# Kernel optimization log

Hardware: AMD Instinct MI355X
Metric: run time of the kernel (lower is better)

## Reference

```python
import jax, jax.numpy as jnp
import numpy as np

STD_MIN = 1e-05
MAX_VAL = 100.0

B, T, C = 16, 8192, 128


def setup_inputs() -> dict:
    key = jax.random.key(0)
    k1, k2 = jax.random.split(key)
    x = jax.random.normal(k1, (B, T, C), dtype=jnp.float32)
    # binary missing-value mask (1 = missing), stored as float per mask.float() in torch
    mask = jax.random.randint(k2, (B, T, C), 0, 2).astype(jnp.float32)
    return {"x": x, "mask": mask}


def reference(x, mask):
    # valid-count running along time: n_t = cumsum(1 - mask)
    nm = 1.0 - mask                      # [B,T,C], 1 where observed
    n = jnp.cumsum(nm, axis=1)
    n = jnp.where(n == 0, 1.0, n)        # avoid div-by-zero before first valid point
    # causal running mean (note: cumsum of x includes masked entries, as in original)
    mean = jax.lax.stop_gradient(jnp.cumsum(x, axis=1) / n)
    # causal running std over masked squared deviations
    std = jnp.sqrt(jnp.cumsum(((x - mean) * nm) ** 2, axis=1) / n)
    std = jnp.where(std > STD_MIN, std, 1.0)
    std = jax.lax.stop_gradient(std)
    return jnp.clip((x - mean) / std, -MAX_VAL, MAX_VAL)
```

## Files before the change

### kernel.cpp

```cpp
#include <hip/hip_runtime.h>
#include <math.h>

constexpr int B = 16;
constexpr int T = 8192;
constexpr int C = 128;
constexpr int CG = C / 4;
constexpr int LSUB = 32;
constexpr int NC = T / LSUB;
constexpr float STD_MIN = 1e-5f;
constexpr float MAX_VAL = 100.0f;

using f32x4 = __attribute__((ext_vector_type(4))) float;

__device__ inline f32x4 sel_neff(f32x4 n) {
    f32x4 r;
    #pragma unroll
    for (int j = 0; j < 4; ++j) r[j] = (n[j] == 0.0f) ? 1.0f : n[j];
    return r;
}
__device__ inline f32x4 rcp4(f32x4 a) {
    f32x4 r;
    #pragma unroll
    for (int j = 0; j < 4; ++j) r[j] = __builtin_amdgcn_rcpf(a[j]);
    return r;
}
__device__ inline f32x4 sqrt4(f32x4 a) {
    f32x4 r;
    #pragma unroll
    for (int j = 0; j < 4; ++j) r[j] = __builtin_amdgcn_sqrtf(a[j]);
    return r;
}
__device__ inline f32x4 decode_nm(unsigned w) {
    f32x4 r;
    #pragma unroll
    for (int j = 0; j < 4; ++j) r[j] = (float)((w >> (8 * j)) & 0xffu);
    return r;
}

__device__ inline void decomp(int gtid, int& b, int& k, int& cg) {
    cg = gtid & (CG - 1);
    k  = (gtid / CG) & (NC - 1);
    b  = gtid / (CG * NC);
}

template <bool BYTES>
__global__ __launch_bounds__(256) void k_pass1(
    const f32x4* __restrict__ x, const f32x4* __restrict__ mask,
    f32x4* __restrict__ sumx, f32x4* __restrict__ sumnm,
    unsigned* __restrict__ nmb)
{
    int gtid = blockIdx.x * 256 + threadIdx.x;
    int b, k, cg; decomp(gtid, b, k, cg);
    size_t base = ((size_t)b * T + (size_t)k * LSUB) * CG + cg;
    f32x4 sx = {0,0,0,0}, sn = {0,0,0,0};
    #pragma unroll 8
    for (int t = 0; t < LSUB; ++t) {
        f32x4 xv = x[base + (size_t)t * CG];
        f32x4 mv = mask[base + (size_t)t * CG];
        f32x4 nm = 1.0f - mv;
        if (BYTES) {
            unsigned w = (unsigned)nm[0] | ((unsigned)nm[1] << 8)
                       | ((unsigned)nm[2] << 16) | ((unsigned)nm[3] << 24);
            nmb[base + (size_t)t * CG] = w;
        }
        sx += xv;
        sn += nm;
    }
    size_t o = ((size_t)b * NC + k) * CG + cg;
    sumx[o]  = sx;
    sumnm[o] = sn;
}

template <int NCOMP>
__device__ inline void block_exscan(float* vals, int lane, int wave)
{
    float inc[NCOMP];
    #pragma unroll
    for (int j = 0; j < NCOMP; ++j) inc[j] = vals[j];
    #pragma unroll
    for (int d = 1; d < 64; d <<= 1) {
        #pragma unroll
        for (int j = 0; j < NCOMP; ++j) {
            float u = __shfl_up(inc[j], d, 64);
            if (lane >= d) inc[j] += u;
        }
    }
    __shared__ float wsum[4][NCOMP];
    if (lane == 63) {
        #pragma unroll
        for (int j = 0; j < NCOMP; ++j) wsum[wave][j] = inc[j];
    }
    __syncthreads();
    float off[NCOMP];
    #pragma unroll
    for (int j = 0; j < NCOMP; ++j) off[j] = 0.0f;
    for (int w = 0; w < wave; ++w) {
        #pragma unroll
        for (int j = 0; j < NCOMP; ++j) off[j] += wsum[w][j];
    }
    #pragma unroll
    for (int j = 0; j < NCOMP; ++j) {
        float e = __shfl_up(inc[j], 1, 64);
        vals[j] = off[j] + ((lane == 0) ? 0.0f : e);
    }
}

__global__ __launch_bounds__(256) void k_scan2(f32x4* __restrict__ a0,
                                               f32x4* __restrict__ a1)
{
    int blk = blockIdx.x, cg = blk & 31, b = blk >> 5;
    int k = threadIdx.x, lane = k & 63, wave = k >> 6;
    size_t o = ((size_t)b * NC + k) * CG + cg;
    f32x4 v0 = a0[o], v1 = a1[o];
    float vals[8] = {v0[0],v0[1],v0[2],v0[3],v1[0],v1[1],v1[2],v1[3]};
    block_exscan<8>(vals, lane, wave);
    a0[o] = (f32x4){vals[0],vals[1],vals[2],vals[3]};
    a1[o] = (f32x4){vals[4],vals[5],vals[6],vals[7]};
}

__global__ __launch_bounds__(256) void k_scan1(f32x4* __restrict__ a0)
{
    int blk = blockIdx.x, cg = blk & 31, b = blk >> 5;
    int k = threadIdx.x, lane = k & 63, wave = k >> 6;
    size_t o = ((size_t)b * NC + k) * CG + cg;
    f32x4 v0 = a0[o];
    float vals[4] = {v0[0],v0[1],v0[2],v0[3]};
    block_exscan<4>(vals, lane, wave);
    a0[o] = (f32x4){vals[0],vals[1],vals[2],vals[3]};
}

template <bool BYTES>
__global__ __launch_bounds__(256) void k_pass3(
    const f32x4* __restrict__ x, const f32x4* __restrict__ mask,
    const unsigned* __restrict__ nmb,
    const f32x4* __restrict__ psumx, const f32x4* __restrict__ psumnm,
    f32x4* __restrict__ sumd2)
{
    int gtid = blockIdx.x * 256 + threadIdx.x;
    int b, k, cg; decomp(gtid, b, k, cg);
    size_t base = ((size_t)b * T + (size_t)k * LSUB) * CG + cg;
    size_t o = ((size_t)b * NC + k) * CG + cg;
    f32x4 rx = psumx[o], rn = psumnm[o];
    f32x4 sd = {0,0,0,0};
    #pragma unroll 8
    for (int t = 0; t < LSUB; ++t) {
        f32x4 xv = x[base + (size_t)t * CG];
        f32x4 nm = BYTES ? decode_nm(nmb[base + (size_t)t * CG])
                         : (1.0f - mask[base + (size_t)t * CG]);
        rx += xv; rn += nm;
        f32x4 mean = rx * rcp4(sel_neff(rn));
        f32x4 d = (xv - mean) * nm;
        sd += d * d;
    }
    sumd2[o] = sd;
}

template <bool BYTES>
__global__ __launch_bounds__(256) void k_pass5(
    const f32x4* __restrict__ x, const f32x4* __restrict__ mask,
    const unsigned* __restrict__ nmb,
    const f32x4* __restrict__ psumx, const f32x4* __restrict__ psumnm,
    const f32x4* __restrict__ psumd2, f32x4* __restrict__ out)
{
    int gtid = blockIdx.x * 256 + threadIdx.x;
    int b, k, cg; decomp(gtid, b, k, cg);
    size_t base = ((size_t)b * T + (size_t)k * LSUB) * CG + cg;
    size_t o = ((size_t)b * NC + k) * CG + cg;
    f32x4 rx = psumx[o], rn = psumnm[o], rd = psumd2[o];
    #pragma unroll 8
    for (int t = 0; t < LSUB; ++t) {
        f32x4 xv = x[base + (size_t)t * CG];
        f32x4 nm = BYTES ? decode_nm(nmb[base + (size_t)t * CG])
                         : (1.0f - mask[base + (size_t)t * CG]);
        rx += xv; rn += nm;
        f32x4 inv = rcp4(sel_neff(rn));
        f32x4 mean = rx * inv;
        f32x4 d = (xv - mean) * nm;
        rd += d * d;
        f32x4 s = sqrt4(rd * inv);
        f32x4 ov;
        #pragma unroll
        for (int j = 0; j < 4; ++j) {
            float invs = (s[j] > STD_MIN) ? __builtin_amdgcn_rcpf(s[j]) : 1.0f;
            float v = (xv[j] - mean[j]) * invs;
            ov[j] = fminf(fmaxf(v, -MAX_VAL), MAX_VAL);
        }
        __builtin_nontemporal_store(ov, &out[base + (size_t)t * CG]);
    }
}

template <bool BYTES>
static void run_all(const f32x4* x, const f32x4* mask, f32x4* out,
                    void* d_ws, hipStream_t stream)
{
    size_t arr_elems = (size_t)B * NC * C;
    f32x4* sumx  = (f32x4*)d_ws;
    f32x4* sumnm = (f32x4*)((float*)d_ws + arr_elems);
    f32x4* sumd2 = (f32x4*)((float*)d_ws + 2 * arr_elems);
    unsigned* nmb = (unsigned*)((float*)d_ws + 3 * arr_elems);

    int main_blocks = B * NC * CG / 256;
    int scan_blocks = B * CG;

    k_pass1<BYTES><<<main_blocks, 256, 0, stream>>>(x, mask, sumx, sumnm, nmb);
    k_scan2<<<scan_blocks, 256, 0, stream>>>(sumx, sumnm);
    k_pass3<BYTES><<<main_blocks, 256, 0, stream>>>(x, mask, nmb, sumx, sumnm, sumd2);
    k_scan1<<<scan_blocks, 256, 0, stream>>>(sumd2);
    k_pass5<BYTES><<<main_blocks, 256, 0, stream>>>(x, mask, nmb, sumx, sumnm, sumd2, out);
}

extern "C" void kernel_launch(void* const* d_in, const int* in_sizes, int n_in,
                              void* d_out, int out_size, void* d_ws, size_t ws_size,
                              hipStream_t stream) {
    const f32x4* x    = (const f32x4*)d_in[0];
    const f32x4* mask = (const f32x4*)d_in[1];
    f32x4* out = (f32x4*)d_out;

    size_t need = 3ull * B * NC * C * sizeof(float)
                + (size_t)B * T * CG * sizeof(unsigned);

    if (ws_size >= need) run_all<true >(x, mask, out, d_ws, stream);
    else                 run_all<false>(x, mask, out, d_ws, stream);
}
```

Before: 87.26 us.

## Split pass1 into tile-cooperative x-sum and mask-sum kernels

Replaces the per-thread strided pass1 with two kernels in which each block covers one 32-step time tile. Threads read contiguous rows and reduce through shared memory, which should make the loads coalesced and better distributed. The mask kernel uses nontemporal loads so the mask stream avoids polluting cache, hoping x stays cached for the next pass. The cost is an extra kernel launch plus a shared-memory reduction and barrier per block.

```diff
diff --git a/kernel.cpp b/kernel.cpp
--- a/kernel.cpp
+++ b/kernel.cpp
@@ -5,8 +5,9 @@
 constexpr int T = 8192;
 constexpr int C = 128;
 constexpr int CG = C / 4;
-constexpr int LSUB = 32;
-constexpr int NC = T / LSUB;
+constexpr int TB = 32;
+constexpr int NC = T / TB;
+constexpr int LSUB = TB;
 constexpr float STD_MIN = 1e-5f;
 constexpr float MAX_VAL = 100.0f;
 
@@ -44,31 +45,56 @@
 }
 
 template <bool BYTES>
-__global__ __launch_bounds__(256) void k_pass1(
-    const f32x4* __restrict__ x, const f32x4* __restrict__ mask,
-    f32x4* __restrict__ sumx, f32x4* __restrict__ sumnm,
+__global__ __launch_bounds__(256) void k_p1a(
+    const f32x4* __restrict__ mask, f32x4* __restrict__ sumnm,
     unsigned* __restrict__ nmb)
 {
-    int gtid = blockIdx.x * 256 + threadIdx.x;
-    int b, k, cg; decomp(gtid, b, k, cg);
-    size_t base = ((size_t)b * T + (size_t)k * LSUB) * CG + cg;
-    f32x4 sx = {0,0,0,0}, sn = {0,0,0,0};
-    #pragma unroll 8
-    for (int t = 0; t < LSUB; ++t) {
-        f32x4 xv = x[base + (size_t)t * CG];
-        f32x4 mv = mask[base + (size_t)t * CG];
+    __shared__ f32x4 p[8][CG];
+    int tid = threadIdx.x, cg = tid & 31, sub = tid >> 5;
+    int blk = blockIdx.x, b = blk >> 8, kb = blk & 255;
+    size_t gbase = (size_t)(b * T + kb * TB) * CG;
+    f32x4 sn = {0,0,0,0};
+    #pragma unroll
+    for (int i = 0; i < 4; ++i) {
+        f32x4 mv;
+        if (BYTES) mv = __builtin_nontemporal_load(&mask[gbase + i * 256 + tid]);
+        else       mv = mask[gbase + i * 256 + tid];
         f32x4 nm = 1.0f - mv;
         if (BYTES) {
             unsigned w = (unsigned)nm[0] | ((unsigned)nm[1] << 8)
                        | ((unsigned)nm[2] << 16) | ((unsigned)nm[3] << 24);
-            nmb[base + (size_t)t * CG] = w;
+            nmb[gbase + i * 256 + tid] = w;
         }
-        sx += xv;
         sn += nm;
     }
-    size_t o = ((size_t)b * NC + k) * CG + cg;
-    sumx[o]  = sx;
-    sumnm[o] = sn;
+    p[sub][cg] = sn;
+    __syncthreads();
+    if (sub == 0) {
+        f32x4 t = p[0][cg];
+        #pragma unroll
+        for (int s = 1; s < 8; ++s) t += p[s][cg];
+        sumnm[((size_t)b * NC + kb) * CG + cg] = t;
+    }
+}
+
+__global__ __launch_bounds__(256) void k_p1b(
+    const f32x4* __restrict__ x, f32x4* __restrict__ sumx)
+{
+    __shared__ f32x4 p[8][CG];
+    int tid = threadIdx.x, cg = tid & 31, sub = tid >> 5;
+    int blk = blockIdx.x, b = blk >> 8, kb = blk & 255;
+    size_t gbase = (size_t)(b * T + kb * TB) * CG;
+    f32x4 sx = {0,0,0,0};
+    #pragma unroll
+    for (int i = 0; i < 4; ++i) sx += x[gbase + i * 256 + tid];
+    p[sub][cg] = sx;
+    __syncthreads();
+    if (sub == 0) {
+        f32x4 t = p[0][cg];
+        #pragma unroll
+        for (int s = 1; s < 8; ++s) t += p[s][cg];
+        sumx[((size_t)b * NC + kb) * CG + cg] = t;
+    }
 }
 
 template <int NCOMP>
@@ -199,10 +225,12 @@
     f32x4* sumd2 = (f32x4*)((float*)d_ws + 2 * arr_elems);
     unsigned* nmb = (unsigned*)((float*)d_ws + 3 * arr_elems);
 
+    int tile_blocks = B * NC;
     int main_blocks = B * NC * CG / 256;
     int scan_blocks = B * CG;
 
-    k_pass1<BYTES><<<main_blocks, 256, 0, stream>>>(x, mask, sumx, sumnm, nmb);
+    k_p1b<<<tile_blocks, 256, 0, stream>>>(x, sumx);
+    k_p1a<BYTES><<<tile_blocks, 256, 0, stream>>>(mask, sumnm, nmb);
     k_scan2<<<scan_blocks, 256, 0, stream>>>(sumx, sumnm);
     k_pass3<BYTES><<<main_blocks, 256, 0, stream>>>(x, mask, nmb, sumx, sumnm, sumd2);
     k_scan1<<<scan_blocks, 256, 0, stream>>>(sumd2);
```

Result: slower. 89.81 us (+2.9%).

## Fuse scans into passes, bit-pack mask, use 128-row chunks per block

Applied to the files above, without the earlier changes.

Replaces the five-kernel pipeline (two passes, two scan kernels, final pass) with three kernels. Each block covers a 128-row time chunk and computes its cross-chunk prefix by summing earlier chunk aggregates directly, so the separate scan kernels go away. The mask is packed to one bit per element in a 64-bit word instead of one byte, cutting mask traffic in the later passes. The cost is redundant prefix reads that grow with the chunk index, extra shared-memory syncs, and holding all 16 rows of x per thread in registers. The workspace-size fallback is removed.

```diff
diff --git a/kernel.cpp b/kernel.cpp
--- a/kernel.cpp
+++ b/kernel.cpp
@@ -1,12 +1,15 @@
 #include <hip/hip_runtime.h>
 #include <math.h>
+#include <stdint.h>
 
 constexpr int B = 16;
 constexpr int T = 8192;
 constexpr int C = 128;
 constexpr int CG = C / 4;
-constexpr int LSUB = 32;
-constexpr int NC = T / LSUB;
+constexpr int TBK = 128;
+constexpr int NCH = T / TBK;
+constexpr int SUBS = 8;
+constexpr int RPT = TBK / SUBS;
 constexpr float STD_MIN = 1e-5f;
 constexpr float MAX_VAL = 100.0f;
 
@@ -30,183 +33,184 @@
     for (int j = 0; j < 4; ++j) r[j] = __builtin_amdgcn_sqrtf(a[j]);
     return r;
 }
-__device__ inline f32x4 decode_nm(unsigned w) {
-    f32x4 r;
-    #pragma unroll
-    for (int j = 0; j < 4; ++j) r[j] = (float)((w >> (8 * j)) & 0xffu);
-    return r;
-}
-
-__device__ inline void decomp(int gtid, int& b, int& k, int& cg) {
-    cg = gtid & (CG - 1);
-    k  = (gtid / CG) & (NC - 1);
-    b  = gtid / (CG * NC);
-}
-
-template <bool BYTES>
-__global__ __launch_bounds__(256) void k_pass1(
+__device__ inline f32x4 decode_nib(unsigned nib) {
+    f32x4 r;
+    r[0] = (float)(nib & 1u);
+    r[1] = (float)((nib >> 1) & 1u);
+    r[2] = (float)((nib >> 2) & 1u);
+    r[3] = (float)((nib >> 3) & 1u);
+    return r;
+}
+
+__global__ __launch_bounds__(256) void k1_sums(
     const f32x4* __restrict__ x, const f32x4* __restrict__ mask,
-    f32x4* __restrict__ sumx, f32x4* __restrict__ sumnm,
-    unsigned* __restrict__ nmb)
+    f32x4* __restrict__ aggx, f32x4* __restrict__ aggn,
+    uint64_t* __restrict__ nmw)
 {
-    int gtid = blockIdx.x * 256 + threadIdx.x;
-    int b, k, cg; decomp(gtid, b, k, cg);
-    size_t base = ((size_t)b * T + (size_t)k * LSUB) * CG + cg;
+    __shared__ f32x4 p0[SUBS][CG], p1[SUBS][CG];
+    int tid = threadIdx.x, cg = tid & 31, sub = tid >> 5;
+    int blk = blockIdx.x, b = blk >> 6, k = blk & (NCH - 1);
+    size_t base = ((size_t)b * T + (size_t)k * TBK + (size_t)sub * RPT) * CG + cg;
+
     f32x4 sx = {0,0,0,0}, sn = {0,0,0,0};
-    #pragma unroll 8
-    for (int t = 0; t < LSUB; ++t) {
-        f32x4 xv = x[base + (size_t)t * CG];
-        f32x4 mv = mask[base + (size_t)t * CG];
+    uint64_t w = 0;
+    #pragma unroll
+    for (int r = 0; r < RPT; ++r) {
+        f32x4 xv = x[base + (size_t)r * CG];
+        f32x4 mv = mask[base + (size_t)r * CG];
         f32x4 nm = 1.0f - mv;
-        if (BYTES) {
-            unsigned w = (unsigned)nm[0] | ((unsigned)nm[1] << 8)
-                       | ((unsigned)nm[2] << 16) | ((unsigned)nm[3] << 24);
-            nmb[base + (size_t)t * CG] = w;
-        }
-        sx += xv;
-        sn += nm;
-    }
-    size_t o = ((size_t)b * NC + k) * CG + cg;
-    sumx[o]  = sx;
-    sumnm[o] = sn;
-}
-
-template <int NCOMP>
-__device__ inline void block_exscan(float* vals, int lane, int wave)
+        sx += xv; sn += nm;
+        unsigned nib = (unsigned)nm[0] | ((unsigned)nm[1] << 1)
+                     | ((unsigned)nm[2] << 2) | ((unsigned)nm[3] << 3);
+        w |= (uint64_t)nib << (4 * r);
+    }
+    nmw[(size_t)blk * 256 + tid] = w;
+    p0[sub][cg] = sx; p1[sub][cg] = sn;
+    __syncthreads();
+    if (sub == 0) {
+        f32x4 tx = p0[0][cg], tn = p1[0][cg];
+        #pragma unroll
+        for (int s = 1; s < SUBS; ++s) { tx += p0[s][cg]; tn += p1[s][cg]; }
+        aggx[(size_t)blk * CG + cg] = tx;
+        aggn[(size_t)blk * CG + cg] = tn;
+    }
+}
+
+__global__ __launch_bounds__(256) void k2_dev2(
+    const f32x4* __restrict__ x,
+    const f32x4* __restrict__ aggx, const f32x4* __restrict__ aggn,
+    const uint64_t* __restrict__ nmw, f32x4* __restrict__ aggd)
 {
-    float inc[NCOMP];
-    #pragma unroll
-    for (int j = 0; j < NCOMP; ++j) inc[j] = vals[j];
-    #pragma unroll
-    for (int d = 1; d < 64; d <<= 1) {
+    __shared__ f32x4 p0[SUBS][CG], p1[SUBS][CG];
+    int tid = threadIdx.x, cg = tid & 31, sub = tid >> 5;
+    int blk = blockIdx.x, b = blk >> 6, k = blk & (NCH - 1);
+    size_t base = ((size_t)b * T + (size_t)k * TBK + (size_t)sub * RPT) * CG + cg;
+
+    f32x4 pxp = {0,0,0,0}, pnp = {0,0,0,0};
+    for (int j = sub; j < k; j += SUBS) {
+        size_t o = ((size_t)(b * NCH + j)) * CG + cg;
+        pxp += aggx[o]; pnp += aggn[o];
+    }
+    p0[sub][cg] = pxp; p1[sub][cg] = pnp;
+    __syncthreads();
+    f32x4 px = p0[0][cg], pn = p1[0][cg];
+    #pragma unroll
+    for (int s = 1; s < SUBS; ++s) { px += p0[s][cg]; pn += p1[s][cg]; }
+
+    f32x4 xr[RPT];
+    #pragma unroll
+    for (int r = 0; r < RPT; ++r) xr[r] = x[base + (size_t)r * CG];
+    uint64_t w = nmw[(size_t)blk * 256 + tid];
+
+    f32x4 sx = {0,0,0,0}, sn = {0,0,0,0};
+    #pragma unroll
+    for (int r = 0; r < RPT; ++r) {
+        sx += xr[r];
+        sn += decode_nib((unsigned)(w >> (4 * r)) & 0xFu);
+    }
+    __syncthreads();
+    p0[sub][cg] = sx; p1[sub][cg] = sn;
+    __syncthreads();
+    f32x4 offx = {0,0,0,0}, offn = {0,0,0,0};
+    for (int s = 0; s < sub; ++s) { offx += p0[s][cg]; offn += p1[s][cg]; }
+
+    f32x4 rx = px + offx, rn = pn + offn, sd = {0,0,0,0};
+    #pragma unroll
+    for (int r = 0; r < RPT; ++r) {
+        f32x4 nm = decode_nib((unsigned)(w >> (4 * r)) & 0xFu);
+        rx += xr[r]; rn += nm;
+        f32x4 mean = rx * rcp4(sel_neff(rn));
+        f32x4 d = (xr[r] - mean) * nm;
+        sd += d * d;
+    }
+    __syncthreads();
+    p0[sub][cg] = sd;
+    __syncthreads();
+    if (sub == 0) {
+        f32x4 td = p0[0][cg];
         #pragma unroll
-        for (int j = 0; j < NCOMP; ++j) {
-            float u = __shfl_up(inc[j], d, 64);
-            if (lane >= d) inc[j] += u;
-        }
-    }
-    __shared__ float wsum[4][NCOMP];
-    if (lane == 63) {
-        #pragma unroll
-        for (int j = 0; j < NCOMP; ++j) wsum[wave][j] = inc[j];
-    }
-    __syncthreads();
-    float off[NCOMP];
-    #pragma unroll
-    for (int j = 0; j < NCOMP; ++j) off[j] = 0.0f;
-    for (int w = 0; w < wave; ++w) {
-        #pragma unroll
-        for (int j = 0; j < NCOMP; ++j) off[j] += wsum[w][j];
-    }
-    #pragma unroll
-    for (int j = 0; j < NCOMP; ++j) {
-        float e = __shfl_up(inc[j], 1, 64);
-        vals[j] = off[j] + ((lane == 0) ? 0.0f : e);
-    }
-}
-
-__global__ __launch_bounds__(256) void k_scan2(f32x4* __restrict__ a0,
-                                               f32x4* __restrict__ a1)
+        for (int s = 1; s < SUBS; ++s) td += p0[s][cg];
+        aggd[(size_t)blk * CG + cg] = td;
+    }
+}
+
+__global__ __launch_bounds__(256) void k3_final(
+    const f32x4* __restrict__ x,
+    const f32x4* __restrict__ aggx, const f32x4* __restrict__ aggn,
+    const f32x4* __restrict__ aggd, const uint64_t* __restrict__ nmw,
+    f32x4* __restrict__ out)
 {
-    int blk = blockIdx.x, cg = blk & 31, b = blk >> 5;
-    int k = threadIdx.x, lane = k & 63, wave = k >> 6;
-    size_t o = ((size_t)b * NC + k) * CG + cg;
-    f32x4 v0 = a0[o], v1 = a1[o];
-    float vals[8] = {v0[0],v0[1],v0[2],v0[3],v1[0],v1[1],v1[2],v1[3]};
-    block_exscan<8>(vals, lane, wave);
-    a0[o] = (f32x4){vals[0],vals[1],vals[2],vals[3]};
-    a1[o] = (f32x4){vals[4],vals[5],vals[6],vals[7]};
-}
-
-__global__ __launch_bounds__(256) void k_scan1(f32x4* __restrict__ a0)
-{
-    int blk = blockIdx.x, cg = blk & 31, b = blk >> 5;
-    int k = threadIdx.x, lane = k & 63, wave = k >> 6;
-    size_t o = ((size_t)b * NC + k) * CG + cg;
-    f32x4 v0 = a0[o];
-    float vals[4] = {v0[0],v0[1],v0[2],v0[3]};
-    block_exscan<4>(vals, lane, wave);
-    a0[o] = (f32x4){vals[0],vals[1],vals[2],vals[3]};
-}
-
-template <bool BYTES>
-__global__ __launch_bounds__(256) void k_pass3(
-    const f32x4* __restrict__ x, const f32x4* __restrict__ mask,
-    const unsigned* __restrict__ nmb,
-    const f32x4* __restrict__ psumx, const f32x4* __restrict__ psumnm,
-    f32x4* __restrict__ sumd2)
-{
-    int gtid = blockIdx.x * 256 + threadIdx.x;
-    int b, k, cg; decomp(gtid, b, k, cg);
-    size_t base = ((size_t)b * T + (size_t)k * LSUB) * CG + cg;
-    size_t o = ((size_t)b * NC + k) * CG + cg;
-    f32x4 rx = psumx[o], rn = psumnm[o];
-    f32x4 sd = {0,0,0,0};
-    #pragma unroll 8
-    for (int t = 0; t < LSUB; ++t) {
-        f32x4 xv = x[base + (size_t)t * CG];
-        f32x4 nm = BYTES ? decode_nm(nmb[base + (size_t)t * CG])
-                         : (1.0f - mask[base + (size_t)t * CG]);
-        rx += xv; rn += nm;
+    __shared__ f32x4 p0[SUBS][CG], p1[SUBS][CG], p2[SUBS][CG];
+    int tid = threadIdx.x, cg = tid & 31, sub = tid >> 5;
+    int blk = blockIdx.x, b = blk >> 6, k = blk & (NCH - 1);
+    size_t base = ((size_t)b * T + (size_t)k * TBK + (size_t)sub * RPT) * CG + cg;
+
+    f32x4 pxp = {0,0,0,0}, pnp = {0,0,0,0}, pdp = {0,0,0,0};
+    for (int j = sub; j < k; j += SUBS) {
+        size_t o = ((size_t)(b * NCH + j)) * CG + cg;
+        pxp += aggx[o]; pnp += aggn[o]; pdp += aggd[o];
+    }
+    p0[sub][cg] = pxp; p1[sub][cg] = pnp; p2[sub][cg] = pdp;
+    __syncthreads();
+    f32x4 px = p0[0][cg], pn = p1[0][cg], pd = p2[0][cg];
+    #pragma unroll
+    for (int s = 1; s < SUBS; ++s) {
+        px += p0[s][cg]; pn += p1[s][cg]; pd += p2[s][cg];
+    }
+
+    f32x4 xr[RPT];
+    #pragma unroll
+    for (int r = 0; r < RPT; ++r) xr[r] = x[base + (size_t)r * CG];
+    uint64_t w = nmw[(size_t)blk * 256 + tid];
+
+    f32x4 sx = {0,0,0,0}, sn = {0,0,0,0};
+    #pragma unroll
+    for (int r = 0; r < RPT; ++r) {
+        sx += xr[r];
+        sn += decode_nib((unsigned)(w >> (4 * r)) & 0xFu);
+    }
+    __syncthreads();
+    p0[sub][cg] = sx; p1[sub][cg] = sn;
+    __syncthreads();
+    f32x4 offx = {0,0,0,0}, offn = {0,0,0,0};
+    for (int s = 0; s < sub; ++s) { offx += p0[s][cg]; offn += p1[s][cg]; }
+    f32x4 rx0 = px + offx, rn0 = pn + offn;
+
+    f32x4 rx = rx0, rn = rn0, sd = {0,0,0,0};
+    #pragma unroll
+    for (int r = 0; r < RPT; ++r) {
+        f32x4 nm = decode_nib((unsigned)(w >> (4 * r)) & 0xFu);
+        rx += xr[r]; rn += nm;
         f32x4 mean = rx * rcp4(sel_neff(rn));
-        f32x4 d = (xv - mean) * nm;
+        f32x4 d = (xr[r] - mean) * nm;
         sd += d * d;
     }
-    sumd2[o] = sd;
-}
-
-template <bool BYTES>
-__global__ __launch_bounds__(256) void k_pass5(
-    const f32x4* __restrict__ x, const f32x4* __restrict__ mask,
-    const unsigned* __restrict__ nmb,
-    const f32x4* __restrict__ psumx, const f32x4* __restrict__ psumnm,
-    const f32x4* __restrict__ psumd2, f32x4* __restrict__ out)
-{
-    int gtid = blockIdx.x * 256 + threadIdx.x;
-    int b, k, cg; decomp(gtid, b, k, cg);
-    size_t base = ((size_t)b * T + (size_t)k * LSUB) * CG + cg;
-    size_t o = ((size_t)b * NC + k) * CG + cg;
-    f32x4 rx = psumx[o], rn = psumnm[o], rd = psumd2[o];
-    #pragma unroll 8
-    for (int t = 0; t < LSUB; ++t) {
-        f32x4 xv = x[base + (size_t)t * CG];
-        f32x4 nm = BYTES ? decode_nm(nmb[base + (size_t)t * CG])
-                         : (1.0f - mask[base + (size_t)t * CG]);
-        rx += xv; rn += nm;
+    __syncthreads();
+    p0[sub][cg] = sd;
+    __syncthreads();
+    f32x4 offd = {0,0,0,0};
+    for (int s = 0; s < sub; ++s) offd += p0[s][cg];
+    f32x4 rd = pd + offd;
+
+    rx = rx0; rn = rn0;
+    #pragma unroll
+    for (int r = 0; r < RPT; ++r) {
+        f32x4 nm = decode_nib((unsigned)(w >> (4 * r)) & 0xFu);
+        rx += xr[r]; rn += nm;
         f32x4 inv = rcp4(sel_neff(rn));
         f32x4 mean = rx * inv;
-        f32x4 d = (xv - mean) * nm;
+        f32x4 d = (xr[r] - mean) * nm;
         rd += d * d;
         f32x4 s = sqrt4(rd * inv);
         f32x4 ov;
         #pragma unroll
         for (int j = 0; j < 4; ++j) {
             float invs = (s[j] > STD_MIN) ? __builtin_amdgcn_rcpf(s[j]) : 1.0f;
-            float v = (xv[j] - mean[j]) * invs;
+            float v = (xr[r][j] - mean[j]) * invs;
             ov[j] = fminf(fmaxf(v, -MAX_VAL), MAX_VAL);
         }
-        __builtin_nontemporal_store(ov, &out[base + (size_t)t * CG]);
-    }
-}
-
-template <bool BYTES>
-static void run_all(const f32x4* x, const f32x4* mask, f32x4* out,
-                    void* d_ws, hipStream_t stream)
-{
-    size_t arr_elems = (size_t)B * NC * C;
-    f32x4* sumx  = (f32x4*)d_ws;
-    f32x4* sumnm = (f32x4*)((float*)d_ws + arr_elems);
-    f32x4* sumd2 = (f32x4*)((float*)d_ws + 2 * arr_elems);
-    unsigned* nmb = (unsigned*)((float*)d_ws + 3 * arr_elems);
-
-    int main_blocks = B * NC * CG / 256;
-    int scan_blocks = B * CG;
-
-    k_pass1<BYTES><<<main_blocks, 256, 0, stream>>>(x, mask, sumx, sumnm, nmb);
-    k_scan2<<<scan_blocks, 256, 0, stream>>>(sumx, sumnm);
-    k_pass3<BYTES><<<main_blocks, 256, 0, stream>>>(x, mask, nmb, sumx, sumnm, sumd2);
-    k_scan1<<<scan_blocks, 256, 0, stream>>>(sumd2);
-    k_pass5<BYTES><<<main_blocks, 256, 0, stream>>>(x, mask, nmb, sumx, sumnm, sumd2, out);
+        __builtin_nontemporal_store(ov, &out[base + (size_t)r * CG]);
+    }
 }
 
 extern "C" void kernel_launch(void* const* d_in, const int* in_sizes, int n_in,
@@ -216,9 +220,15 @@
     const f32x4* mask = (const f32x4*)d_in[1];
     f32x4* out = (f32x4*)d_out;
 
-    size_t need = 3ull * B * NC * C * sizeof(float)
-                + (size_t)B * T * CG * sizeof(unsigned);
-
-    if (ws_size >= need) run_all<true >(x, mask, out, d_ws, stream);
-    else                 run_all<false>(x, mask, out, d_ws, stream);
-}
+    size_t agg_elems = (size_t)B * NCH * CG;
+    f32x4* aggx = (f32x4*)d_ws;
+    f32x4* aggn = aggx + agg_elems;
+    f32x4* aggd = aggn + agg_elems;
+    uint64_t* nmw = (uint64_t*)(aggd + agg_elems);
+
+    int grid = B * NCH;
+
+    k1_sums<<<grid, 256, 0, stream>>>(x, mask, aggx, aggn, nmw);
+    k2_dev2<<<grid, 256, 0, stream>>>(x, aggx, aggn, nmw, aggd);
+    k3_final<<<grid, 256, 0, stream>>>(x, aggx, aggn, aggd, nmw, out);
+}
```

Result: faster. 72.94 us (-16.4%).
